# Optimization experiments

Hardware: AMD Instinct MI355X
Metric: run time of the kernel (lower is better)

The kernel has to match this reference:

```python
import jax, jax.numpy as jnp
import numpy as np

EPS = 1e-6  # model.epsilon


def setup_inputs() -> dict:
    key = jax.random.key(0)
    k1, k2 = jax.random.split(key)
    # X: one-hot-like translated sequence tensor [genomes, tiles, 6 frames, tile_len, alphabet]
    X = jax.random.uniform(k1, (8, 12, 6, 2000, 21), dtype=jnp.float32)
    Q = jnp.full((21,), 1.0 / 21.0, dtype=jnp.float32)  # background aa distribution
    # P_logit initialized like log(Q) + noise (matches _getRandomProfiles)
    P_logit = jnp.log(Q)[None, :, None] + 4.0 * jax.random.normal(k2, (8, 21, 48), dtype=jnp.float32)
    return {"X": X, "P_logit": P_logit, "Q": Q}


def reference(X, P_logit, Q):
    # P = softmax over alphabet axis; R = log odds vs background, clamped at epsilon
    P = jax.nn.softmax(P_logit, axis=1)                      # [k, A, U]
    R = jnp.log(jnp.maximum(P / Q[None, :, None], EPS))      # [k, A, U]
    D0, D1, D2, L, A = X.shape
    k, _, U = R.shape
    # conv2d with spatial (L, A), in_ch 1, out_ch U; width window covers full alphabet
    Xr = X.reshape(D0 * D1 * D2, L, A, 1)
    W = R.reshape(k, A, 1, U)
    Z = jax.lax.conv_general_dilated(
        Xr, W, window_strides=(1, 1), padding='VALID',
        dimension_numbers=('NHWC', 'HWIO', 'NHWC'))          # [B, L-k+1, 1, U]
    Z = Z.reshape(D0, D1, D2, L - k + 1, U)                  # [D0, D1, D2, P, U]
    S = jnp.max(Z, axis=(2, 3))                              # max over frames & positions -> [D0, D1, U]
    return (S, R, Z)
```

## Files before the change

kernel.cpp:

```cpp
#include <hip/hip_runtime.h>
#include <math.h>

typedef __attribute__((ext_vector_type(8))) short short8;
typedef __attribute__((ext_vector_type(4))) float f32x4;

#define D0n 8
#define D1n 12
#define D2n 6
#define Ln 2000
#define An 21
#define KPn 8
#define Un 48
#define PPn 1993
#define Bn 576
#define Gn 96
#define S_SIZE 4608
#define R_SIZE 8064

#define BPn 256
#define NPT 8
#define XROWS 264
#define XS_BYTES (XROWS * 64)
#define RB_BYTES (384 * 64)
#define RED_OFF (XS_BYTES + RB_BYTES)

__device__ __forceinline__ int swz(int b) { return b ^ ((b >> 2) & 0x70); }

__device__ __forceinline__ unsigned int fkey(float f) {
    unsigned int u = __float_as_uint(f);
    return (u & 0x80000000u) ? ~u : (u | 0x80000000u);
}
__device__ __forceinline__ float funkey(unsigned int k) {
    return __uint_as_float((k & 0x80000000u) ? (k ^ 0x80000000u) : ~k);
}
__device__ __forceinline__ unsigned short f2bf(float v) {
    unsigned int b = __float_as_uint(v);
    return (unsigned short)((b + 0x7FFFu + ((b >> 16) & 1u)) >> 16);
}

#define GLOAD_LDS16(g, l)                                                     \
    __builtin_amdgcn_global_load_lds(                                          \
        (const __attribute__((address_space(1))) void*)(g),                    \
        (__attribute__((address_space(3))) void*)(l), 16, 0, 0)

__global__ void k_profile(const float* __restrict__ P_logit,
                          const float* __restrict__ Q,
                          float* __restrict__ Rout,
                          unsigned short* __restrict__ Rb,
                          unsigned int* __restrict__ Skey) {
    int t = blockIdx.x * blockDim.x + threadIdx.x;
    if (t < S_SIZE) Skey[t] = 0u;
    if (t >= KPn * Un) return;
    int kp = t / Un, u = t % Un;
    const float* pl = P_logit + kp * (An * Un) + u;
    float v[An];
    float m = -INFINITY;
#pragma unroll
    for (int a = 0; a < An; ++a) { v[a] = pl[a * Un]; m = fmaxf(m, v[a]); }
    float s = 0.f;
#pragma unroll
    for (int a = 0; a < An; ++a) { v[a] = expf(v[a] - m); s += v[a]; }
    float inv = 1.f / s;
    int rowp = kp * Un + u;
#pragma unroll
    for (int a = 0; a < An; ++a) {
        float r = logf(fmaxf(v[a] * inv / Q[a], 1e-6f));
        Rout[(kp * An + a) * Un + u] = r;
        Rb[swz(rowp * 64 + a * 2) >> 1] = f2bf(r);
    }
#pragma unroll
    for (int a = An; a < 32; ++a) Rb[swz(rowp * 64 + a * 2) >> 1] = 0;
}

__global__ __launch_bounds__(512) void k_conv(const float* __restrict__ X,
                                              const unsigned short* __restrict__ Rb,
                                              float* __restrict__ Z,
                                              unsigned int* __restrict__ Skey) {
    __shared__ char smem[XS_BYTES + RB_BYTES + 8 * Un * 4];
    const int b = blockIdx.y;
    const int p0 = blockIdx.x * BPn;
    const int t = threadIdx.x;

    {
        const uint4* src = (const uint4*)Rb;
        uint4* dst = (uint4*)(smem + XS_BYTES);
#pragma unroll
        for (int i = 0; i < RB_BYTES / 16 / 512; ++i) {
            int idx = t + i * 512;
            GLOAD_LDS16(src + idx, dst + idx);
        }
    }
    {
        uint4 z4 = {0u, 0u, 0u, 0u};
        uint4* xs = (uint4*)smem;
        for (int i = t; i < XS_BYTES / 16; i += 512) xs[i] = z4;
    }
    __syncthreads();
    {
        const int rows_avail = min(XROWS, Ln - p0);
        const int npair = rows_avail * 11;
        const float* Xb = X + ((size_t)b * Ln + p0) * An;
        for (int j = t; j < npair; j += 512) {
            int row = j / 11, jj = j - row * 11;
            int a = jj * 2;
            float v0 = Xb[row * An + a];
            float v1 = (a + 1 < An) ? Xb[row * An + a + 1] : 0.f;
            unsigned int pk = (unsigned int)f2bf(v0) |
                              ((unsigned int)f2bf(v1) << 16);
            *(unsigned int*)(smem + swz(row * 64 + a * 2)) = pk;
        }
    }
    __syncthreads();

    const int w = t >> 6;
    const int l = t & 63;
    const int lr = l & 15;
    const int ls = l >> 4;
    const int pw = w * 32;

    f32x4 acc[2][3];
#pragma unroll
    for (int m = 0; m < 2; ++m)
#pragma unroll
        for (int n = 0; n < 3; ++n) acc[m][n] = (f32x4){0.f, 0.f, 0.f, 0.f};

#pragma unroll
    for (int q = 0; q < KPn; ++q) {
        const int ar = pw + q + lr;
        short8 a0 = *(const short8*)(smem + swz(ar * 64 + ls * 16));
        short8 a1 = *(const short8*)(smem + swz((ar + 16) * 64 + ls * 16));
        const int br = q * Un + lr;
        short8 b0 = *(const short8*)(smem + XS_BYTES + swz(br * 64 + ls * 16));
        short8 b1 = *(const short8*)(smem + XS_BYTES + swz((br + 16) * 64 + ls * 16));
        short8 b2 = *(const short8*)(smem + XS_BYTES + swz((br + 32) * 64 + ls * 16));
        acc[0][0] = __builtin_amdgcn_mfma_f32_16x16x32_bf16(a0, b0, acc[0][0], 0, 0, 0);
        acc[0][1] = __builtin_amdgcn_mfma_f32_16x16x32_bf16(a0, b1, acc[0][1], 0, 0, 0);
        acc[0][2] = __builtin_amdgcn_mfma_f32_16x16x32_bf16(a0, b2, acc[0][2], 0, 0, 0);
        acc[1][0] = __builtin_amdgcn_mfma_f32_16x16x32_bf16(a1, b0, acc[1][0], 0, 0, 0);
        acc[1][1] = __builtin_amdgcn_mfma_f32_16x16x32_bf16(a1, b1, acc[1][1], 0, 0, 0);
        acc[1][2] = __builtin_amdgcn_mfma_f32_16x16x32_bf16(a1, b2, acc[1][2], 0, 0, 0);
    }

    float tmax[3] = {-INFINITY, -INFINITY, -INFINITY};
#pragma unroll
    for (int m = 0; m < 2; ++m) {
#pragma unroll
        for (int r = 0; r < 4; ++r) {
            int p = p0 + pw + m * 16 + ls * 4 + r;
            if (p < PPn) {
                float* zp = Z + ((size_t)b * PPn + p) * Un + lr;
#pragma unroll
                for (int n = 0; n < 3; ++n) {
                    float val = acc[m][n][r];
                    zp[n * 16] = val;
                    tmax[n] = fmaxf(tmax[n], val);
                }
            }
        }
    }

#pragma unroll
    for (int n = 0; n < 3; ++n) {
        tmax[n] = fmaxf(tmax[n], __shfl_xor(tmax[n], 16));
        tmax[n] = fmaxf(tmax[n], __shfl_xor(tmax[n], 32));
    }
    float* red = (float*)(smem + RED_OFF);
    if (ls == 0) {
#pragma unroll
        for (int n = 0; n < 3; ++n) red[w * Un + n * 16 + lr] = tmax[n];
    }
    __syncthreads();
    if (t < Un) {
        float m = -INFINITY;
#pragma unroll
        for (int wv = 0; wv < 8; ++wv) m = fmaxf(m, red[wv * Un + t]);
        atomicMax(&Skey[(b / D2n) * Un + t], fkey(m));
    }
}

__global__ void k_decode(unsigned int* __restrict__ Skey) {
    int t = blockIdx.x * blockDim.x + threadIdx.x;
    if (t < S_SIZE) {
        float f = funkey(Skey[t]);
        ((float*)Skey)[t] = f;
    }
}

extern "C" void kernel_launch(void* const* d_in, const int* in_sizes, int n_in,
                              void* d_out, int out_size, void* d_ws, size_t ws_size,
                              hipStream_t stream) {
    const float* X = (const float*)d_in[0];
    const float* P_logit = (const float*)d_in[1];
    const float* Q = (const float*)d_in[2];

    float* S = (float*)d_out;
    float* Rout = S + S_SIZE;
    float* Z = Rout + R_SIZE;
    unsigned short* Rb = (unsigned short*)d_ws;

    k_profile<<<(S_SIZE + 63) / 64, 64, 0, stream>>>(P_logit, Q, Rout, Rb,
                                                     (unsigned int*)d_out);

    dim3 grid(NPT, Bn);
    k_conv<<<grid, 512, 0, stream>>>(X, Rb, Z, (unsigned int*)d_out);

    k_decode<<<(S_SIZE + 255) / 256, 256, 0, stream>>>((unsigned int*)d_out);
}
```

Baseline: 101.8 us.

## Keep profile weights in registers and halve conv block size

```diff
diff --git a/kernel.cpp b/kernel.cpp
--- a/kernel.cpp
+++ b/kernel.cpp
@@ -13,16 +13,14 @@
 #define Un 48
 #define PPn 1993
 #define Bn 576
-#define Gn 96
 #define S_SIZE 4608
 #define R_SIZE 8064
 
-#define BPn 256
-#define NPT 8
-#define XROWS 264
+#define BPn 128
+#define NPT 16
+#define XROWS 136
 #define XS_BYTES (XROWS * 64)
-#define RB_BYTES (384 * 64)
-#define RED_OFF (XS_BYTES + RB_BYTES)
+#define RED_OFF XS_BYTES
 
 __device__ __forceinline__ int swz(int b) { return b ^ ((b >> 2) & 0x70); }
 
@@ -37,11 +35,6 @@
     unsigned int b = __float_as_uint(v);
     return (unsigned short)((b + 0x7FFFu + ((b >> 16) & 1u)) >> 16);
 }
-
-#define GLOAD_LDS16(g, l)                                                     \
-    __builtin_amdgcn_global_load_lds(                                          \
-        (const __attribute__((address_space(1))) void*)(g),                    \
-        (__attribute__((address_space(3))) void*)(l), 16, 0, 0)
 
 __global__ void k_profile(const float* __restrict__ P_logit,
                           const float* __restrict__ Q,
@@ -72,35 +65,46 @@
     for (int a = An; a < 32; ++a) Rb[swz(rowp * 64 + a * 2) >> 1] = 0;
 }
 
-__global__ __launch_bounds__(512) void k_conv(const float* __restrict__ X,
-                                              const unsigned short* __restrict__ Rb,
-                                              float* __restrict__ Z,
-                                              unsigned int* __restrict__ Skey) {
-    __shared__ char smem[XS_BYTES + RB_BYTES + 8 * Un * 4];
+__global__ __launch_bounds__(256, 3) void k_conv(
+        const float* __restrict__ X,
+        const unsigned short* __restrict__ Rb,
+        float* __restrict__ Z,
+        unsigned int* __restrict__ Skey) {
+    __shared__ char smem[XS_BYTES + 4 * Un * 4];
     const int b = blockIdx.y;
     const int p0 = blockIdx.x * BPn;
     const int t = threadIdx.x;
-
-    {
-        const uint4* src = (const uint4*)Rb;
-        uint4* dst = (uint4*)(smem + XS_BYTES);
-#pragma unroll
-        for (int i = 0; i < RB_BYTES / 16 / 512; ++i) {
-            int idx = t + i * 512;
-            GLOAD_LDS16(src + idx, dst + idx);
-        }
-    }
+    const int w = t >> 6;
+    const int l = t & 63;
+    const int lr = l & 15;
+    const int ls = l >> 4;
+    const int pw = w * 32;
+
+    short8 bf[KPn][3];
+#pragma unroll
+    for (int q = 0; q < KPn; ++q)
+#pragma unroll
+        for (int nt = 0; nt < 3; ++nt) {
+            int rowp = q * Un + nt * 16 + lr;
+            bf[q][nt] = *(const short8*)((const char*)Rb +
+                                         swz(rowp * 64 + ls * 16));
+        }
+
     {
         uint4 z4 = {0u, 0u, 0u, 0u};
         uint4* xs = (uint4*)smem;
-        for (int i = t; i < XS_BYTES / 16; i += 512) xs[i] = z4;
+#pragma unroll
+        for (int i = 0; i < XS_BYTES / 16 / 256 + 1; ++i) {
+            int idx = t + i * 256;
+            if (idx < XS_BYTES / 16) xs[idx] = z4;
+        }
     }
     __syncthreads();
     {
         const int rows_avail = min(XROWS, Ln - p0);
         const int npair = rows_avail * 11;
         const float* Xb = X + ((size_t)b * Ln + p0) * An;
-        for (int j = t; j < npair; j += 512) {
+        for (int j = t; j < npair; j += 256) {
             int row = j / 11, jj = j - row * 11;
             int a = jj * 2;
             float v0 = Xb[row * An + a];
@@ -112,12 +116,6 @@
     }
     __syncthreads();
 
-    const int w = t >> 6;
-    const int l = t & 63;
-    const int lr = l & 15;
-    const int ls = l >> 4;
-    const int pw = w * 32;
-
     f32x4 acc[2][3];
 #pragma unroll
     for (int m = 0; m < 2; ++m)
@@ -129,16 +127,12 @@
         const int ar = pw + q + lr;
         short8 a0 = *(const short8*)(smem + swz(ar * 64 + ls * 16));
         short8 a1 = *(const short8*)(smem + swz((ar + 16) * 64 + ls * 16));
-        const int br = q * Un + lr;
-        short8 b0 = *(const short8*)(smem + XS_BYTES + swz(br * 64 + ls * 16));
-        short8 b1 = *(const short8*)(smem + XS_BYTES + swz((br + 16) * 64 + ls * 16));
-        short8 b2 = *(const short8*)(smem + XS_BYTES + swz((br + 32) * 64 + ls * 16));
-        acc[0][0] = __builtin_amdgcn_mfma_f32_16x16x32_bf16(a0, b0, acc[0][0], 0, 0, 0);
-        acc[0][1] = __builtin_amdgcn_mfma_f32_16x16x32_bf16(a0, b1, acc[0][1], 0, 0, 0);
-        acc[0][2] = __builtin_amdgcn_mfma_f32_16x16x32_bf16(a0, b2, acc[0][2], 0, 0, 0);
-        acc[1][0] = __builtin_amdgcn_mfma_f32_16x16x32_bf16(a1, b0, acc[1][0], 0, 0, 0);
-        acc[1][1] = __builtin_amdgcn_mfma_f32_16x16x32_bf16(a1, b1, acc[1][1], 0, 0, 0);
-        acc[1][2] = __builtin_amdgcn_mfma_f32_16x16x32_bf16(a1, b2, acc[1][2], 0, 0, 0);
+        acc[0][0] = __builtin_amdgcn_mfma_f32_16x16x32_bf16(a0, bf[q][0], acc[0][0], 0, 0, 0);
+        acc[0][1] = __builtin_amdgcn_mfma_f32_16x16x32_bf16(a0, bf[q][1], acc[0][1], 0, 0, 0);
+        acc[0][2] = __builtin_amdgcn_mfma_f32_16x16x32_bf16(a0, bf[q][2], acc[0][2], 0, 0, 0);
+        acc[1][0] = __builtin_amdgcn_mfma_f32_16x16x32_bf16(a1, bf[q][0], acc[1][0], 0, 0, 0);
+        acc[1][1] = __builtin_amdgcn_mfma_f32_16x16x32_bf16(a1, bf[q][1], acc[1][1], 0, 0, 0);
+        acc[1][2] = __builtin_amdgcn_mfma_f32_16x16x32_bf16(a1, bf[q][2], acc[1][2], 0, 0, 0);
     }
 
     float tmax[3] = {-INFINITY, -INFINITY, -INFINITY};
@@ -173,7 +167,7 @@
     if (t < Un) {
         float m = -INFINITY;
 #pragma unroll
-        for (int wv = 0; wv < 8; ++wv) m = fmaxf(m, red[wv * Un + t]);
+        for (int wv = 0; wv < 4; ++wv) m = fmaxf(m, red[wv * Un + t]);
         atomicMax(&Skey[(b / D2n) * Un + t], fkey(m));
     }
 }
@@ -202,7 +196,7 @@
                                                      (unsigned int*)d_out);
 
     dim3 grid(NPT, Bn);
-    k_conv<<<grid, 512, 0, stream>>>(X, Rb, Z, (unsigned int*)d_out);
+    k_conv<<<grid, 256, 0, stream>>>(X, Rb, Z, (unsigned int*)d_out);
 
     k_decode<<<(S_SIZE + 255) / 256, 256, 0, stream>>>((unsigned int*)d_out);
 }
```

Result: slower. 126.9 us (+24.7%).

## Loop four position tiles per block with double-buffered X prefetch and vector Z stores

Applied to the files above, without the earlier changes.

```diff
diff --git a/kernel.cpp b/kernel.cpp
--- a/kernel.cpp
+++ b/kernel.cpp
@@ -13,16 +13,16 @@
 #define Un 48
 #define PPn 1993
 #define Bn 576
-#define Gn 96
 #define S_SIZE 4608
 #define R_SIZE 8064
 
 #define BPn 256
-#define NPT 8
+#define TILES 4
 #define XROWS 264
-#define XS_BYTES (XROWS * 64)
+#define XBUF_BYTES (XROWS * 64)
 #define RB_BYTES (384 * 64)
-#define RED_OFF (XS_BYTES + RB_BYTES)
+#define BOFF (2 * XBUF_BYTES)
+#define RED_OFF (BOFF + RB_BYTES)
 
 __device__ __forceinline__ int swz(int b) { return b ^ ((b >> 2) & 0x70); }
 
@@ -72,103 +72,153 @@
     for (int a = An; a < 32; ++a) Rb[swz(rowp * 64 + a * 2) >> 1] = 0;
 }
 
-__global__ __launch_bounds__(512) void k_conv(const float* __restrict__ X,
-                                              const unsigned short* __restrict__ Rb,
-                                              float* __restrict__ Z,
-                                              unsigned int* __restrict__ Skey) {
-    __shared__ char smem[XS_BYTES + RB_BYTES + 8 * Un * 4];
+__device__ __forceinline__ void xwrite4(char* xbase, int idx, f32x4 g) {
+    int fi = idx * 4;
+    int row = fi / An;
+    int a = fi - row * An;
+#pragma unroll
+    for (int e = 0; e < 4; ++e) {
+        *(unsigned short*)(xbase + swz(row * 64 + a * 2)) = f2bf(g[e]);
+        ++a;
+        if (a == An) { a = 0; ++row; }
+    }
+}
+
+__global__ __launch_bounds__(512) void k_conv(
+        const float* __restrict__ X,
+        const unsigned short* __restrict__ Rb,
+        float* __restrict__ Z,
+        unsigned int* __restrict__ Skey) {
+    __shared__ char smem[2 * XBUF_BYTES + RB_BYTES + 8 * Un * 4];
     const int b = blockIdx.y;
-    const int p0 = blockIdx.x * BPn;
+    const int base_p = blockIdx.x * (TILES * BPn);
     const int t = threadIdx.x;
-
-    {
-        const uint4* src = (const uint4*)Rb;
-        uint4* dst = (uint4*)(smem + XS_BYTES);
-#pragma unroll
-        for (int i = 0; i < RB_BYTES / 16 / 512; ++i) {
-            int idx = t + i * 512;
-            GLOAD_LDS16(src + idx, dst + idx);
-        }
-    }
-    {
-        uint4 z4 = {0u, 0u, 0u, 0u};
-        uint4* xs = (uint4*)smem;
-        for (int i = t; i < XS_BYTES / 16; i += 512) xs[i] = z4;
-    }
-    __syncthreads();
-    {
-        const int rows_avail = min(XROWS, Ln - p0);
-        const int npair = rows_avail * 11;
-        const float* Xb = X + ((size_t)b * Ln + p0) * An;
-        for (int j = t; j < npair; j += 512) {
-            int row = j / 11, jj = j - row * 11;
-            int a = jj * 2;
-            float v0 = Xb[row * An + a];
-            float v1 = (a + 1 < An) ? Xb[row * An + a + 1] : 0.f;
-            unsigned int pk = (unsigned int)f2bf(v0) |
-                              ((unsigned int)f2bf(v1) << 16);
-            *(unsigned int*)(smem + swz(row * 64 + a * 2)) = pk;
-        }
-    }
-    __syncthreads();
-
     const int w = t >> 6;
     const int l = t & 63;
     const int lr = l & 15;
     const int ls = l >> 4;
     const int pw = w * 32;
 
-    f32x4 acc[2][3];
-#pragma unroll
-    for (int m = 0; m < 2; ++m)
-#pragma unroll
-        for (int n = 0; n < 3; ++n) acc[m][n] = (f32x4){0.f, 0.f, 0.f, 0.f};
-
-#pragma unroll
-    for (int q = 0; q < KPn; ++q) {
-        const int ar = pw + q + lr;
-        short8 a0 = *(const short8*)(smem + swz(ar * 64 + ls * 16));
-        short8 a1 = *(const short8*)(smem + swz((ar + 16) * 64 + ls * 16));
-        const int br = q * Un + lr;
-        short8 b0 = *(const short8*)(smem + XS_BYTES + swz(br * 64 + ls * 16));
-        short8 b1 = *(const short8*)(smem + XS_BYTES + swz((br + 16) * 64 + ls * 16));
-        short8 b2 = *(const short8*)(smem + XS_BYTES + swz((br + 32) * 64 + ls * 16));
-        acc[0][0] = __builtin_amdgcn_mfma_f32_16x16x32_bf16(a0, b0, acc[0][0], 0, 0, 0);
-        acc[0][1] = __builtin_amdgcn_mfma_f32_16x16x32_bf16(a0, b1, acc[0][1], 0, 0, 0);
-        acc[0][2] = __builtin_amdgcn_mfma_f32_16x16x32_bf16(a0, b2, acc[0][2], 0, 0, 0);
-        acc[1][0] = __builtin_amdgcn_mfma_f32_16x16x32_bf16(a1, b0, acc[1][0], 0, 0, 0);
-        acc[1][1] = __builtin_amdgcn_mfma_f32_16x16x32_bf16(a1, b1, acc[1][1], 0, 0, 0);
-        acc[1][2] = __builtin_amdgcn_mfma_f32_16x16x32_bf16(a1, b2, acc[1][2], 0, 0, 0);
-    }
-
-    float tmax[3] = {-INFINITY, -INFINITY, -INFINITY};
-#pragma unroll
-    for (int m = 0; m < 2; ++m) {
-#pragma unroll
-        for (int r = 0; r < 4; ++r) {
-            int p = p0 + pw + m * 16 + ls * 4 + r;
+    {
+        const uint4* src = (const uint4*)Rb;
+        uint4* dst = (uint4*)(smem + BOFF);
+#pragma unroll
+        for (int i = 0; i < RB_BYTES / 16 / 512; ++i) {
+            int idx = t + i * 512;
+            GLOAD_LDS16(src + idx, dst + idx);
+        }
+    }
+    {
+        uint4 z4 = {0u, 0u, 0u, 0u};
+        uint4* xs = (uint4*)smem;
+        for (int i = t; i < 2 * XBUF_BYTES / 16; i += 512) xs[i] = z4;
+    }
+    const float* Xb = X + ((size_t)b * Ln + base_p) * An;
+    f32x4 g[3];
+    int n4_0;
+    {
+        int rows = min(XROWS, Ln - base_p);
+        n4_0 = rows * An / 4;
+        const f32x4* src = (const f32x4*)Xb;
+#pragma unroll
+        for (int i = 0; i < 3; ++i) {
+            int idx = t + i * 512;
+            g[i] = (idx < n4_0) ? src[idx] : (f32x4){0.f, 0.f, 0.f, 0.f};
+        }
+    }
+    __syncthreads();
+#pragma unroll
+    for (int i = 0; i < 3; ++i) {
+        int idx = t + i * 512;
+        if (idx < n4_0) xwrite4((char*)smem, idx, g[i]);
+    }
+    __syncthreads();
+
+    float smax[3][4];
+#pragma unroll
+    for (int nu = 0; nu < 3; ++nu)
+#pragma unroll
+        for (int r = 0; r < 4; ++r) smax[nu][r] = -INFINITY;
+
+    int n4_next = 0;
+    for (int tt = 0; tt < TILES; ++tt) {
+        char* xb = (char*)smem + (tt & 1) * XBUF_BYTES;
+        const int tp0 = base_p + tt * BPn;
+
+        if (tt + 1 < TILES) {
+            int np0 = base_p + (tt + 1) * BPn;
+            int rows = min(XROWS, Ln - np0);
+            n4_next = rows * An / 4;
+            const f32x4* src = (const f32x4*)(X + ((size_t)b * Ln + np0) * An);
+#pragma unroll
+            for (int i = 0; i < 3; ++i) {
+                int idx = t + i * 512;
+                g[i] = (idx < n4_next) ? src[idx] : (f32x4){0.f, 0.f, 0.f, 0.f};
+            }
+        }
+
+        f32x4 acc[3][2];
+#pragma unroll
+        for (int nu = 0; nu < 3; ++nu)
+#pragma unroll
+            for (int np = 0; np < 2; ++np) acc[nu][np] = (f32x4){0.f, 0.f, 0.f, 0.f};
+
+#pragma unroll
+        for (int q = 0; q < KPn; ++q) {
+            const int rr = q * Un + lr;
+            short8 rf0 = *(const short8*)(smem + BOFF + swz(rr * 64 + ls * 16));
+            short8 rf1 = *(const short8*)(smem + BOFF + swz((rr + 16) * 64 + ls * 16));
+            short8 rf2 = *(const short8*)(smem + BOFF + swz((rr + 32) * 64 + ls * 16));
+            const int xr = pw + q + lr;
+            short8 xf0 = *(const short8*)(xb + swz(xr * 64 + ls * 16));
+            short8 xf1 = *(const short8*)(xb + swz((xr + 16) * 64 + ls * 16));
+            acc[0][0] = __builtin_amdgcn_mfma_f32_16x16x32_bf16(rf0, xf0, acc[0][0], 0, 0, 0);
+            acc[0][1] = __builtin_amdgcn_mfma_f32_16x16x32_bf16(rf0, xf1, acc[0][1], 0, 0, 0);
+            acc[1][0] = __builtin_amdgcn_mfma_f32_16x16x32_bf16(rf1, xf0, acc[1][0], 0, 0, 0);
+            acc[1][1] = __builtin_amdgcn_mfma_f32_16x16x32_bf16(rf1, xf1, acc[1][1], 0, 0, 0);
+            acc[2][0] = __builtin_amdgcn_mfma_f32_16x16x32_bf16(rf2, xf0, acc[2][0], 0, 0, 0);
+            acc[2][1] = __builtin_amdgcn_mfma_f32_16x16x32_bf16(rf2, xf1, acc[2][1], 0, 0, 0);
+        }
+
+#pragma unroll
+        for (int np = 0; np < 2; ++np) {
+            int p = tp0 + pw + np * 16 + lr;
             if (p < PPn) {
-                float* zp = Z + ((size_t)b * PPn + p) * Un + lr;
-#pragma unroll
-                for (int n = 0; n < 3; ++n) {
-                    float val = acc[m][n][r];
-                    zp[n * 16] = val;
-                    tmax[n] = fmaxf(tmax[n], val);
+                float* zp = Z + ((size_t)b * PPn + p) * Un + ls * 4;
+#pragma unroll
+                for (int nu = 0; nu < 3; ++nu) {
+                    *(f32x4*)(zp + nu * 16) = acc[nu][np];
+#pragma unroll
+                    for (int r = 0; r < 4; ++r)
+                        smax[nu][r] = fmaxf(smax[nu][r], acc[nu][np][r]);
                 }
             }
         }
-    }
-
-#pragma unroll
-    for (int n = 0; n < 3; ++n) {
-        tmax[n] = fmaxf(tmax[n], __shfl_xor(tmax[n], 16));
-        tmax[n] = fmaxf(tmax[n], __shfl_xor(tmax[n], 32));
-    }
+
+        if (tt + 1 < TILES) {
+            __syncthreads();
+            char* xn = (char*)smem + ((tt + 1) & 1) * XBUF_BYTES;
+#pragma unroll
+            for (int i = 0; i < 3; ++i) {
+                int idx = t + i * 512;
+                if (idx < n4_next) xwrite4(xn, idx, g[i]);
+            }
+            __syncthreads();
+        }
+    }
+
     float* red = (float*)(smem + RED_OFF);
-    if (ls == 0) {
-#pragma unroll
-        for (int n = 0; n < 3; ++n) red[w * Un + n * 16 + lr] = tmax[n];
-    }
+#pragma unroll
+    for (int nu = 0; nu < 3; ++nu)
+#pragma unroll
+        for (int r = 0; r < 4; ++r) {
+            float v = smax[nu][r];
+            v = fmaxf(v, __shfl_xor(v, 1));
+            v = fmaxf(v, __shfl_xor(v, 2));
+            v = fmaxf(v, __shfl_xor(v, 4));
+            v = fmaxf(v, __shfl_xor(v, 8));
+            if (lr == 0) red[w * Un + nu * 16 + ls * 4 + r] = v;
+        }
     __syncthreads();
     if (t < Un) {
         float m = -INFINITY;
@@ -201,7 +251,7 @@
     k_profile<<<(S_SIZE + 63) / 64, 64, 0, stream>>>(P_logit, Q, Rout, Rb,
                                                      (unsigned int*)d_out);
 
-    dim3 grid(NPT, Bn);
+    dim3 grid(2, Bn);
     k_conv<<<grid, 512, 0, stream>>>(X, Rb, Z, (unsigned int*)d_out);
 
     k_decode<<<(S_SIZE + 255) / 256, 256, 0, stream>>>((unsigned int*)d_out);
```

Result: faster. 88.34 us (-13.2%).
